# Optimization experiments

Measured on AMD Instinct MI355X. Metric: run time of the kernel, lower is better.

## Reference

```python
import jax, jax.numpy as jnp
import numpy as np

N_NODES = 50000
N_EDGES = 800000
IN_CH = 64
OUT_CH = 128
N_HEADS = 4
HEAD_DIM = OUT_CH // N_HEADS
LN_EPS = 1e-5


def setup_inputs() -> dict:
    key = jax.random.key(0)
    ks = jax.random.split(key, 12)
    def lin(k, fan_in, fan_out):
        bound = 1.0 / np.sqrt(fan_in)
        kw, kb = jax.random.split(k)
        W = jax.random.uniform(kw, (fan_in, fan_out), jnp.float32, -bound, bound)
        b = jax.random.uniform(kb, (fan_out,), jnp.float32, -bound, bound)
        return W, b
    Wq, bq = lin(ks[0], IN_CH, OUT_CH)
    Wk, bk = lin(ks[1], IN_CH, OUT_CH)
    Wv, bv = lin(ks[2], IN_CH, OUT_CH)
    We1, be1 = lin(ks[3], 2 * IN_CH, OUT_CH)
    We2, be2 = lin(ks[4], OUT_CH, N_HEADS)
    Wo, bo = lin(ks[5], OUT_CH, OUT_CH)
    gamma = jnp.ones((OUT_CH,), jnp.float32)
    beta = jnp.zeros((OUT_CH,), jnp.float32)
    x = jax.random.normal(ks[6], (N_NODES, IN_CH), jnp.float32)
    edge_index = jax.random.randint(ks[7], (2, N_EDGES), 0, N_NODES, jnp.int64 if jax.config.jax_enable_x64 else jnp.int32)
    return {"x": x, "edge_index": edge_index,
            "Wq": Wq, "bq": bq, "Wk": Wk, "bk": bk, "Wv": Wv, "bv": bv,
            "We1": We1, "be1": be1, "We2": We2, "be2": be2,
            "Wo": Wo, "bo": bo, "gamma": gamma, "beta": beta}


def reference(x, edge_index, Wq, bq, Wk, bk, Wv, bv, We1, be1, We2, be2, Wo, bo, gamma, beta):
    # Projections -> [N, H, Dh]
    q = (x @ Wq + bq).reshape(-1, N_HEADS, HEAD_DIM)
    k = (x @ Wk + bk).reshape(-1, N_HEADS, HEAD_DIM)
    v = (x @ Wv + bv).reshape(-1, N_HEADS, HEAD_DIM)
    src, dst = edge_index[0], edge_index[1]
    # Edge MLP attention weights: [E, H, 1]
    edge_features = jnp.concatenate([x[src], x[dst]], axis=-1)  # [E, 2*IN_CH]
    edge_weights = jax.nn.relu(edge_features @ We1 + be1) @ We2 + be2  # [E, H]
    edge_weights = edge_weights[:, :, None]
    # Attention logits per edge: [E, H, 1]
    attn = jnp.sum(q[dst] * k[src], axis=-1, keepdims=True)
    attn = attn * edge_weights / np.sqrt(HEAD_DIM).astype(np.float32)
    # Faithful to original: softmax over the edge dimension (dim=0)
    attn = jax.nn.softmax(attn, axis=0)
    # Weighted gather-scatter aggregation: [N, H, Dh]
    out = jax.ops.segment_sum(attn * v[src], dst, num_segments=N_NODES)
    out = out.reshape(-1, OUT_CH)
    # Output transform (dropout is identity in eval mode) + LayerNorm
    out = out @ Wo + bo
    mu = jnp.mean(out, axis=-1, keepdims=True)
    var = jnp.var(out, axis=-1, keepdims=True)
    out = (out - mu) * jax.lax.rsqrt(var + LN_EPS) * gamma + beta
    return out
```

## Files before the change

### kernel.cpp

```cpp
#include <hip/hip_runtime.h>
#include <hip/hip_bf16.h>

typedef __hip_bfloat16 bf16;
typedef __attribute__((ext_vector_type(8))) short short8;
typedef __attribute__((ext_vector_type(4))) float f32x4;
typedef __attribute__((ext_vector_type(2))) float f32x2;
typedef _Float16 h2 __attribute__((ext_vector_type(2)));

constexpr int NN = 50000;
constexpr int NE = 800000;
constexpr int IC = 64;
constexpr int OC = 128;
constexpr int NH = 4;
constexpr unsigned F32_ONE = 0x3F800000u;
constexpr float KC = 0.25503486f;

__device__ __forceinline__ float ldf(const void* p, int i, bool f32) {
    return f32 ? ((const float*)p)[i]
               : __bfloat162float(((const bf16*)p)[i]);
}

__device__ __forceinline__ int ld_idx(const void* p, long long i, bool i64) {
    return i64 ? (int)((const long long*)p)[i] : ((const int*)p)[i];
}

__device__ __forceinline__ bool probe_i64(const void* ei) {
    const unsigned* u = (const unsigned*)ei;
    return (u[1] | u[3] | u[5] | u[7]) == 0u;
}

__device__ __forceinline__ unsigned f2bu(float x) {
    unsigned u = __float_as_uint(x);
    return (u + 0x7FFFu + ((u >> 16) & 1u)) >> 16;
}

__device__ __forceinline__ h2 u2h(unsigned u) { return __builtin_bit_cast(h2, u); }

__device__ __forceinline__ float fdot2(h2 a, h2 b, float c) {
#if __has_builtin(__builtin_amdgcn_fdot2)
    return __builtin_amdgcn_fdot2(a, b, c, false);
#else
    return c + (float)a[0] * (float)b[0] + (float)a[1] * (float)b[1];
#endif
}

__device__ __forceinline__ h2 relu2(h2 a) {
    h2 z = {(_Float16)0.f, (_Float16)0.f};
#if __has_builtin(__builtin_elementwise_max)
    return __builtin_elementwise_max(a, z);
#else
    h2 r;
    r[0] = a[0] > (_Float16)0.f ? a[0] : (_Float16)0.f;
    r[1] = a[1] > (_Float16)0.f ? a[1] : (_Float16)0.f;
    return r;
#endif
}

#define DPPADD(x, ctrl) \
    ((x) + __int_as_float(__builtin_amdgcn_mov_dpp(__float_as_int(x), (ctrl), 0xF, 0xF, false)))

__device__ __forceinline__ int rfl(int v) { return __builtin_amdgcn_readfirstlane(v); }

__device__ __forceinline__ unsigned char f32_to_fp8(float x) {
#if __has_builtin(__builtin_amdgcn_cvt_pk_fp8_f32)
    return (unsigned char)(__builtin_amdgcn_cvt_pk_fp8_f32(x, x, 0, false) & 0xFF);
#else
    unsigned bits = __float_as_uint(x);
    unsigned s = bits >> 31;
    float a = fabsf(x);
    if (a >= 448.f) return (unsigned char)((s << 7) | 0x7E);
    if (a < 0.015625f) {
        int m = (int)(a * 512.f + 0.5f);
        if (m >= 8) return (unsigned char)((s << 7) | 0x08);
        return (unsigned char)((s << 7) | m);
    }
    unsigned ab = (bits & 0x7FFFFFFFu) + 0x00080000u;
    int e8 = (int)(ab >> 23) - 127 + 7;
    unsigned m3 = (ab >> 20) & 7u;
    if (e8 >= 16) return (unsigned char)((s << 7) | 0x7E);
    return (unsigned char)((s << 7) | ((unsigned)e8 << 3) | m3);
#endif
}

__device__ __forceinline__ void fp8x2_to_f32(unsigned u, float& f0, float& f1) {
#if __has_builtin(__builtin_amdgcn_cvt_pk_f32_fp8)
    f32x2 lo = __builtin_amdgcn_cvt_pk_f32_fp8(u, false);
    f0 = lo[0]; f1 = lo[1];
#else
    float r[2];
#pragma unroll
    for (int j = 0; j < 2; ++j) {
        unsigned b = (u >> (8 * j)) & 0xFF;
        unsigned s = b >> 7, e = (b >> 3) & 15, m = b & 7;
        float v = (e == 0) ? (float)m * 0.001953125f
                           : __uint_as_float(((e + 120u) << 23) | (m << 20));
        r[j] = s ? -v : v;
    }
    f0 = r[0]; f1 = r[1];
#endif
}

constexpr int PB_X   = 12500;
constexpr int PB_W   = 160;
constexpr int PB_WO  = 64;
constexpr int PB_CNT = 3125;

__global__ __launch_bounds__(256) void prep(
    const void* __restrict__ x,
    const void* __restrict__ Wq, const void* __restrict__ bq,
    const void* __restrict__ Wk, const void* __restrict__ bk,
    const void* __restrict__ Wv, const void* __restrict__ bv,
    const void* __restrict__ We1, const void* __restrict__ be1,
    const void* __restrict__ We2, const void* __restrict__ be2,
    const void* __restrict__ Wo,  const unsigned* __restrict__ gw,
    const void* __restrict__ eia, const void* __restrict__ eib, int split,
    bf16* __restrict__ xb, bf16* __restrict__ WcatT, bf16* __restrict__ WoT,
    int* __restrict__ cnt, int* __restrict__ rank,
    unsigned* __restrict__ We2h, float* __restrict__ be2f,
    float* __restrict__ bcat)
{
    const bool f32 = (gw[0] == F32_ONE);
    int b = blockIdx.x, t = threadIdx.x;
    if (b < PB_X) {
        int i = b * 256 + t;
        if (i < NN * IC) xb[i] = __float2bfloat16(ldf(x, i, f32));
    } else if (b < PB_X + PB_W) {
        int idx = (b - PB_X) * 256 + t;
        int n = idx >> 6, k = idx & 63;
        int sel = n >> 7, c = n & 127;
        float v;
        if (sel == 0)      v = ldf(Wq, k * OC + c, f32);
        else if (sel == 1) v = ldf(Wk, k * OC + c, f32);
        else if (sel == 2) v = ldf(Wv, k * OC + c, f32);
        else if (sel == 3) v = ldf(We1, k * OC + c, f32);
        else               v = ldf(We1, (IC + k) * OC + c, f32);
        WcatT[idx] = __float2bfloat16(v);
    } else if (b < PB_X + PB_W + PB_WO) {
        int idx = (b - PB_X - PB_W) * 256 + t;
        int n = idx >> 7, k = idx & 127;
        WoT[idx] = __float2bfloat16(ldf(Wo, k * OC + n, f32));
    } else if (b < PB_X + PB_W + PB_WO + PB_CNT) {
        const bool i64 = probe_i64(eia);
        long long e = (long long)(b - PB_X - PB_W - PB_WO) * 256 + t;
        int d = split ? ld_idx(eib, e, i64) : ld_idx(eia, NE + e, i64);
        int r = atomicAdd(&cnt[d], 1);
        rank[e] = r;
    } else {
        if (t < NH) be2f[t] = ldf(be2, t, f32);
        {
            int ln = t >> 2, k = t & 3;
            int g = ln >> 4, ii = ln & 15;
            int pp = 4 * ii + k;
            h2 hv;
            hv[0] = (_Float16)ldf(We2, (2 * pp) * NH + g, f32);
            hv[1] = (_Float16)ldf(We2, (2 * pp + 1) * NH + g, f32);
            We2h[t] = __builtin_bit_cast(unsigned, hv);
        }
        for (int n = t; n < 5 * OC; n += 256) {
            int sel = n >> 7, c = n & 127;
            float bb = 0.f;
            if (sel == 0) bb = ldf(bq, c, f32);
            else if (sel == 1) bb = ldf(bk, c, f32);
            else if (sel == 2) bb = ldf(bv, c, f32);
            else if (sel == 4) bb = ldf(be1, c, f32);
            bcat[n] = bb;
        }
    }
}

constexpr int SCAN_NB = 49;

__global__ __launch_bounds__(256) void scan_part(const int* __restrict__ cnt,
                                                 int* __restrict__ bsum,
                                                 int* __restrict__ rowptr)
{
    int b = blockIdx.x, t = threadIdx.x;
    int base = b * 1024 + t * 4;
    int4 v;
    if (base < NN) v = *(const int4*)(cnt + base);
    else { v.x = 0; v.y = 0; v.z = 0; v.w = 0; }
    int s = v.x + v.y + v.z + v.w;
#pragma unroll
    for (int off = 1; off < 64; off <<= 1) s += __shfl_xor(s, off);
    __shared__ int sm[4];
    int lane = t & 63, w = t >> 6;
    if (lane == 0) sm[w] = s;
    __syncthreads();
    if (t == 0) bsum[b] = sm[0] + sm[1] + sm[2] + sm[3];
    if (b == 0 && t == 0) rowptr[NN] = NE;
}

__global__ __launch_bounds__(256) void scan_fin(const int* __restrict__ cnt,
                                                const int* __restrict__ bsum,
                                                int* __restrict__ rowptr)
{
    int b = blockIdx.x, t = threadIdx.x;
    int lane = t & 63, w = t >> 6;
    __shared__ int s_boff;
    __shared__ int wsum[4];
    if (w == 0) {
        int pre = (lane < b) ? bsum[lane] : 0;
#pragma unroll
        for (int off = 1; off < 64; off <<= 1) pre += __shfl_xor(pre, off);
        if (lane == 0) s_boff = pre;
    }
    int base = b * 1024 + t * 4;
    int4 v;
    if (base < NN) v = *(const int4*)(cnt + base);
    else { v.x = 0; v.y = 0; v.z = 0; v.w = 0; }
    int s = v.x + v.y + v.z + v.w;
    int inc = s;
#pragma unroll
    for (int off = 1; off < 64; off <<= 1) {
        int u = __shfl_up(inc, off);
        if (lane >= off) inc += u;
    }
    if (lane == 63) wsum[w] = inc;
    __syncthreads();
    int run = s_boff + (inc - s);
#pragma unroll
    for (int i = 0; i < 3; ++i) if (i < w) run += wsum[i];
    if (base < NN) {
        int4 rp;
        rp.x = run;
        rp.y = rp.x + v.x;
        rp.z = rp.y + v.y;
        rp.w = rp.z + v.z;
        *(int4*)(rowptr + base) = rp;
    }
}

constexpr int NG_GEMM = 3125;
constexpr int NG_FILL = 3125;

__global__ __launch_bounds__(256) void node_gemm(
    const bf16* __restrict__ xb, const bf16* __restrict__ WcatT,
    const float* __restrict__ bcat,
    unsigned char* __restrict__ qb_dst, unsigned char* __restrict__ ka_src,
    unsigned char* __restrict__ vf8,
    const void* __restrict__ eia, const void* __restrict__ eib, int split,
    const int* __restrict__ rowptr, const int* __restrict__ rank,
    int* __restrict__ ssrc)
{
    __shared__ _Float16 qbs[16][264];
    __shared__ _Float16 kas[16][264];
    __shared__ unsigned char vfs[16][144];

    if (blockIdx.x >= NG_GEMM) {
        const bool i64 = probe_i64(eia);
        long long e = (long long)(blockIdx.x - NG_GEMM) * 256 + threadIdx.x;
        int s = ld_idx(eia, e, i64);
        int d = split ? ld_idx(eib, e, i64) : ld_idx(eia, NE + e, i64);
        int pos = rowptr[d] + rank[e];
        ssrc[pos] = s;
        return;
    }
    int wave = threadIdx.x >> 6;
    int lane = threadIdx.x & 63;
    int quad = lane >> 4;
    int l16  = lane & 15;
    int row_base = blockIdx.x * 16;
    int m = row_base + l16;

    short8 a0 = *(const short8*)(xb + (size_t)m * IC + quad * 8);
    short8 a1 = *(const short8*)(xb + (size_t)m * IC + 32 + quad * 8);

#pragma unroll
    for (int t = 0; t < 10; ++t) {
        int colbase = wave * 160 + t * 16;
        const bf16* bp = WcatT + (size_t)(colbase + l16) * IC + quad * 8;
        short8 b0 = *(const short8*)(bp);
        short8 b1 = *(const short8*)(bp + 32);
        f32x4 acc = {0.f, 0.f, 0.f, 0.f};
        acc = __builtin_amdgcn_mfma_f32_16x16x32_bf16(a0, b0, acc, 0, 0, 0);
        acc = __builtin_amdgcn_mfma_f32_16x16x32_bf16(a1, b1, acc, 0, 0, 0);

        float bias = bcat[colbase + l16];
        int sel = colbase >> 7;
        int cc  = (colbase & 127) + l16;
#pragma unroll
        for (int r = 0; r < 4; ++r) {
            int l = quad * 4 + r;
            float fv = acc[r] + bias;
            if (sel == 2) {
                vfs[l][cc] = f32_to_fp8(fv);
            } else {
                _Float16 val = (_Float16)fv;
                if (sel == 0)      qbs[l][cc] = val;
                else if (sel == 1) kas[l][cc] = val;
                else if (sel == 3) kas[l][128 + cc] = val;
                else               qbs[l][128 + cc] = val;
            }
        }
    }
    __syncthreads();

    int tix = threadIdx.x;
#pragma unroll
    for (int j = 0; j < 2; ++j) {
        int i = tix + j * 256;
        int row = i >> 5, idx = i & 31;
        *(uint4*)(qb_dst + (size_t)(row_base + row) * 512 + idx * 16) =
            *(const uint4*)((const char*)&qbs[row][0] + idx * 16);
        *(uint4*)(ka_src + (size_t)(row_base + row) * 512 + idx * 16) =
            *(const uint4*)((const char*)&kas[row][0] + idx * 16);
    }
    if (tix < 128) {
        int row = tix >> 3, idx = tix & 7;
        *(uint4*)(vf8 + (size_t)(row_base + row) * OC + idx * 16) =
            *(const uint4*)((const char*)&vfs[row][0] + idx * 16);
    }
}

__global__ __launch_bounds__(256) void edge_gather(
    const int* __restrict__ rowptr, const int* __restrict__ ssrc,
    unsigned char* __restrict__ qb_dst, const unsigned char* __restrict__ ka_src,
    const unsigned char* __restrict__ vf8,
    const unsigned* __restrict__ We2h, const float* __restrict__ be2f,
    float* __restrict__ spart)
{
    int node = rfl(blockIdx.x * 4 + (threadIdx.x >> 6));
    int lane = threadIdx.x & 63;
    int i16  = lane & 15;
    int myh  = lane >> 4;

    const unsigned char* drow = qb_dst + (size_t)node * 512;
    h2 dq = u2h(*(const unsigned*)(drow + lane * 4));
    uint4 dbu = *(const uint4*)(drow + 256 + 16 * i16);
    h2 db0 = u2h(dbu.x), db1 = u2h(dbu.y), db2 = u2h(dbu.z), db3 = u2h(dbu.w);

    uint4 wu = *(const uint4*)(We2h + lane * 4);
    h2 w0 = u2h(wu.x), w1 = u2h(wu.y), w2 = u2h(wu.z), w3 = u2h(wu.w);
    float be2h = be2f[myh];

    int beg = rfl(rowptr[node]);
    int end = rfl(rowptr[node + 1]);
    float o0 = 0.f, o1 = 0.f, s_acc = 0.f;

    if (beg < end) {
        int ib = (beg + 1 < end) ? beg + 1 : end - 1;
        int sa = rfl(ssrc[beg]);
        int sb = rfl(ssrc[ib]);
        const unsigned char* ra = ka_src + (size_t)sa * 512;
        const unsigned char* rb = ka_src + (size_t)sb * 512;
        unsigned kuA = *(const unsigned*)(ra + lane * 4);
        uint4    auA = *(const uint4*)(ra + 256 + 16 * i16);
        unsigned uvA = *(const unsigned short*)(vf8 + (size_t)sa * OC + 2 * lane);
        unsigned kuB = *(const unsigned*)(rb + lane * 4);
        uint4    auB = *(const uint4*)(rb + 256 + 16 * i16);
        unsigned uvB = *(const unsigned short*)(vf8 + (size_t)sb * OC + 2 * lane);
        int na = (beg + 2 < end) ? beg + 2 : end - 1;
        int nb = (beg + 3 < end) ? beg + 3 : end - 1;
        int sna = rfl(ssrc[na]);
        int snb = rfl(ssrc[nb]);

        for (int p = beg; p < end; p += 2) {
            const unsigned char* rc = ka_src + (size_t)sna * 512;
            const unsigned char* rd = ka_src + (size_t)snb * 512;
            unsigned kuC = *(const unsigned*)(rc + lane * 4);
            uint4    auC = *(const uint4*)(rc + 256 + 16 * i16);
            unsigned uvC = *(const unsigned short*)(vf8 + (size_t)sna * OC + 2 * lane);
            unsigned kuD = *(const unsigned*)(rd + lane * 4);
            uint4    auD = *(const uint4*)(rd + 256 + 16 * i16);
            unsigned uvD = *(const unsigned short*)(vf8 + (size_t)snb * OC + 2 * lane);
            int fa = (p + 4 < end) ? p + 4 : end - 1;
            int fb = (p + 5 < end) ? p + 5 : end - 1;
            int s4a = rfl(ssrc[fa]);
            int s4b = rfl(ssrc[fb]);

            bool hasB = (p + 1 < end);

            float tA = fdot2(u2h(kuA), dq, 0.f);
            float tB = fdot2(u2h(kuB), dq, 0.f);
            h2 hA0 = relu2(u2h(auA.x) + db0);
            h2 hA1 = relu2(u2h(auA.y) + db1);
            h2 hA2 = relu2(u2h(auA.z) + db2);
            h2 hA3 = relu2(u2h(auA.w) + db3);
            h2 hB0 = relu2(u2h(auB.x) + db0);
            h2 hB1 = relu2(u2h(auB.y) + db1);
            h2 hB2 = relu2(u2h(auB.z) + db2);
            h2 hB3 = relu2(u2h(auB.w) + db3);
            float pA = fdot2(hA3, w3, fdot2(hA2, w2, fdot2(hA1, w1, fdot2(hA0, w0, 0.f))));
            float pB = fdot2(hB3, w3, fdot2(hB2, w2, fdot2(hB1, w1, fdot2(hB0, w0, 0.f))));

            tA = DPPADD(tA, 0xB1);  pA = DPPADD(pA, 0xB1);
            tB = DPPADD(tB, 0xB1);  pB = DPPADD(pB, 0xB1);
            tA = DPPADD(tA, 0x4E);  pA = DPPADD(pA, 0x4E);
            tB = DPPADD(tB, 0x4E);  pB = DPPADD(pB, 0x4E);
            tA = DPPADD(tA, 0x128); pA = DPPADD(pA, 0x128);
            tB = DPPADD(tB, 0x128); pB = DPPADD(pB, 0x128);
            tA = DPPADD(tA, 0x124); pA = DPPADD(pA, 0x124);
            tB = DPPADD(tB, 0x124); pB = DPPADD(pB, 0x124);

            float coefA = exp2f(tA * (pA + be2h) * KC);
            float coefB = hasB ? exp2f(tB * (pB + be2h) * KC) : 0.f;
            s_acc += coefA + coefB;

            float vA0, vA1, vB0, vB1;
            fp8x2_to_f32(uvA, vA0, vA1);
            fp8x2_to_f32(uvB, vB0, vB1);
            o0 = fmaf(coefA, vA0, fmaf(coefB, vB0, o0));
            o1 = fmaf(coefA, vA1, fmaf(coefB, vB1, o1));

            kuA = kuC; auA = auC; uvA = uvC;
            kuB = kuD; auB = auD; uvB = uvD;
            sna = s4a; snb = s4b;
        }
    }
    *(unsigned*)(qb_dst + (size_t)node * 512 + lane * 4) = f2bu(o0) | (f2bu(o1) << 16);
    if (i16 == 0) spart[node * 4 + myh] = s_acc;
}

constexpr int SR_BLOCKS = 98;
__global__ __launch_bounds__(256) void s_reduce(const float* __restrict__ spart,
                                                float* __restrict__ ssum)
{
    int tid = blockIdx.x * 256 + threadIdx.x;
    int h = threadIdx.x & 3;
    float s = 0.f;
    for (int i = tid; i < NN * 4; i += SR_BLOCKS * 256) s += spart[i];
#pragma unroll
    for (int off = 4; off <= 32; off <<= 1) s += __shfl_xor(s, off);
    __shared__ float sm[4][4];
    int lane = threadIdx.x & 63, w = threadIdx.x >> 6;
    if (lane < 4) sm[w][h] = s;
    __syncthreads();
    if (threadIdx.x < 4) {
        float tot = sm[0][h] + sm[1][h] + sm[2][h] + sm[3][h];
        atomicAdd(&ssum[h], tot);
    }
}

__global__ __launch_bounds__(256) void out_gemm(
    const unsigned char* __restrict__ aggv, const bf16* __restrict__ WoT,
    const void* __restrict__ bo, const void* __restrict__ gamma,
    const void* __restrict__ beta, const unsigned* __restrict__ gw,
    const float* __restrict__ ssum,
    void* __restrict__ out)
{
    const bool f32 = (gw[0] == F32_ONE);
    int wave = threadIdx.x >> 6;
    int lane = threadIdx.x & 63;
    int quad = lane >> 4;
    int l16  = lane & 15;
    int rb = blockIdx.x * 64 + wave * 16;
    int m = rb + l16;
    int ma = (m < NN) ? m : 0;

    const bf16* arow = (const bf16*)(aggv + (size_t)ma * 512);
    short8 a[4];
#pragma unroll
    for (int h = 0; h < 4; ++h) {
        short8 raw = *(const short8*)(arow + h * 32 + quad * 8);
        float invh = 1.0f / ssum[h];
#pragma unroll
        for (int jj = 0; jj < 8; ++jj) {
            float f = __uint_as_float(((unsigned)(unsigned short)raw[jj]) << 16) * invh;
            raw[jj] = (short)f2bu(f);
        }
        a[h] = raw;
    }

    float o[8][4];
#pragma unroll
    for (int t = 0; t < 8; ++t) {
        const bf16* bp = WoT + (size_t)(t * 16 + l16) * OC + quad * 8;
        f32x4 acc = {0.f, 0.f, 0.f, 0.f};
#pragma unroll
        for (int h = 0; h < 4; ++h) {
            short8 bfr = *(const short8*)(bp + h * 32);
            acc = __builtin_amdgcn_mfma_f32_16x16x32_bf16(a[h], bfr, acc, 0, 0, 0);
        }
        float bias = ldf(bo, t * 16 + l16, f32);
#pragma unroll
        for (int r = 0; r < 4; ++r) o[t][r] = acc[r] + bias;
    }

#pragma unroll
    for (int r = 0; r < 4; ++r) {
        float s1 = 0.f, s2 = 0.f;
#pragma unroll
        for (int t = 0; t < 8; ++t) { s1 += o[t][r]; s2 += o[t][r] * o[t][r]; }
#pragma unroll
        for (int off = 1; off <= 8; off <<= 1) {
            s1 += __shfl_xor(s1, off);
            s2 += __shfl_xor(s2, off);
        }
        float mu = s1 * (1.0f / OC);
        float var = fmaxf(s2 * (1.0f / OC) - mu * mu, 0.f);
        float rs = rsqrtf(var + 1e-5f);
        int node = rb + quad * 4 + r;
        if (node < NN) {
#pragma unroll
            for (int t = 0; t < 8; ++t) {
                int col = t * 16 + l16;
                float y = (o[t][r] - mu) * rs * ldf(gamma, col, f32) + ldf(beta, col, f32);
                if (f32) ((float*)out)[(size_t)node * OC + col] = y;
                else     ((bf16*)out)[(size_t)node * OC + col] = __float2bfloat16(y);
            }
        }
    }
}

extern "C" void kernel_launch(void* const* d_in, const int* in_sizes, int n_in,
                              void* d_out, int out_size, void* d_ws, size_t ws_size,
                              hipStream_t stream)
{
    int p = 0;
    const void* x   = d_in[p++];
    const void* eia = d_in[p++];
    const void* eib = eia;
    int split = 0;
    if (n_in >= 17) { eib = d_in[p++]; split = 1; }
    const void* Wq   = d_in[p++];
    const void* bq   = d_in[p++];
    const void* Wk   = d_in[p++];
    const void* bk   = d_in[p++];
    const void* Wv   = d_in[p++];
    const void* bv   = d_in[p++];
    const void* We1  = d_in[p++];
    const void* be1  = d_in[p++];
    const void* We2  = d_in[p++];
    const void* be2  = d_in[p++];
    const void* Wo   = d_in[p++];
    const void* bo   = d_in[p++];
    const void* gamma= d_in[p++];
    const void* beta = d_in[p++];
    const unsigned* gw = (const unsigned*)gamma;

    char* w = (char*)d_ws;
    bf16*  xb     = (bf16*)w;                  w += (size_t)NN * IC * 2;
    unsigned char* qb_dst = (unsigned char*)w; w += (size_t)NN * 512;
    unsigned char* ka_src = (unsigned char*)w; w += (size_t)NN * 512;
    unsigned char* vf8    = (unsigned char*)w; w += (size_t)NN * OC;
    int*   ssrc   = (int*)w;                   w += (size_t)NE * 4;
    int*   rank   = (int*)w;                   w += (size_t)NE * 4;
    int*   cnt    = (int*)w;                   w += (size_t)NN * 4;
    float* ssum   = (float*)w;                 w += 8 * 4;
    int*   rowptr = (int*)w;                   w += (size_t)(NN + 4) * 4;
    int*   bsum   = (int*)w;                   w += 64 * 4;
    float* spart  = (float*)w;                 w += (size_t)NN * 4 * 4;
    unsigned* We2h = (unsigned*)w;             w += 256 * 4;
    float* be2f   = (float*)w;                 w += NH * 4;
    bf16*  WcatT  = (bf16*)w;                  w += (size_t)5 * OC * IC * 2;
    float* bcat   = (float*)w;                 w += 5 * OC * 4;
    bf16*  WoT    = (bf16*)w;                  w += (size_t)OC * OC * 2;

    if (ws_size < (size_t)((char*)w - (char*)d_ws)) return;

    hipMemsetAsync(cnt, 0, (size_t)NN * 4 + 32, stream);
    prep<<<PB_X + PB_W + PB_WO + PB_CNT + 1, 256, 0, stream>>>(
        x, Wq, bq, Wk, bk, Wv, bv, We1, be1, We2, be2, Wo, gw,
        eia, eib, split,
        xb, WcatT, WoT, cnt, rank, We2h, be2f, bcat);
    scan_part<<<SCAN_NB, 256, 0, stream>>>(cnt, bsum, rowptr);
    scan_fin<<<SCAN_NB, 256, 0, stream>>>(cnt, bsum, rowptr);
    node_gemm<<<NG_GEMM + NG_FILL, 256, 0, stream>>>(
        xb, WcatT, bcat, qb_dst, ka_src, vf8, eia, eib, split, rowptr, rank, ssrc);
    edge_gather<<<NN / 4, 256, 0, stream>>>(rowptr, ssrc, qb_dst, ka_src, vf8,
                                            We2h, be2f, spart);
    s_reduce<<<SR_BLOCKS, 256, 0, stream>>>(spart, ssum);
    out_gemm<<<(NN + 63) / 64, 256, 0, stream>>>(qb_dst, WoT, bo, gamma, beta, gw,
                                                 ssum, d_out);
}
```

Baseline: 286.2 us.

## Fuse x bf16 conversion into node GEMM and use inline DPP adds

The separate prep pass that converted x to a bf16 buffer is removed. The node GEMM now loads x directly and converts fp32 to bf16 in registers, which saves a full write and re-read of the converted node features. The DPP cross-lane reductions in the edge gather are also rewritten as inline-asm v_add_f32 with DPP modifiers, so each step becomes one fused instruction instead of a mov_dpp followed by an add. The inline asm carries some risk around missing wait states for DPP hazards.

```diff
diff --git a/kernel.cpp b/kernel.cpp
--- a/kernel.cpp
+++ b/kernel.cpp
@@ -56,10 +56,23 @@
 #endif
 }
 
-#define DPPADD(x, ctrl) \
-    ((x) + __int_as_float(__builtin_amdgcn_mov_dpp(__float_as_int(x), (ctrl), 0xF, 0xF, false)))
+#define DPPFADD(x, ctrl) \
+    asm("v_add_f32 %0, %0, %0 " ctrl " row_mask:0xf bank_mask:0xf" : "+v"(x))
 
 __device__ __forceinline__ int rfl(int v) { return __builtin_amdgcn_readfirstlane(v); }
+
+__device__ __forceinline__ short8 ld_xrow(const void* x, bool f32, int m, int off) {
+    if (!f32) return *(const short8*)((const bf16*)x + (size_t)m * IC + off);
+    const float* xr = (const float*)x + (size_t)m * IC + off;
+    float4 u0 = *(const float4*)xr;
+    float4 u1 = *(const float4*)(xr + 4);
+    short8 r;
+    r[0] = (short)f2bu(u0.x); r[1] = (short)f2bu(u0.y);
+    r[2] = (short)f2bu(u0.z); r[3] = (short)f2bu(u0.w);
+    r[4] = (short)f2bu(u1.x); r[5] = (short)f2bu(u1.y);
+    r[6] = (short)f2bu(u1.z); r[7] = (short)f2bu(u1.w);
+    return r;
+}
 
 __device__ __forceinline__ unsigned char f32_to_fp8(float x) {
 #if __has_builtin(__builtin_amdgcn_cvt_pk_fp8_f32)
@@ -100,13 +113,11 @@
 #endif
 }
 
-constexpr int PB_X   = 12500;
 constexpr int PB_W   = 160;
 constexpr int PB_WO  = 64;
 constexpr int PB_CNT = 3125;
 
 __global__ __launch_bounds__(256) void prep(
-    const void* __restrict__ x,
     const void* __restrict__ Wq, const void* __restrict__ bq,
     const void* __restrict__ Wk, const void* __restrict__ bk,
     const void* __restrict__ Wv, const void* __restrict__ bv,
@@ -114,18 +125,15 @@
     const void* __restrict__ We2, const void* __restrict__ be2,
     const void* __restrict__ Wo,  const unsigned* __restrict__ gw,
     const void* __restrict__ eia, const void* __restrict__ eib, int split,
-    bf16* __restrict__ xb, bf16* __restrict__ WcatT, bf16* __restrict__ WoT,
+    bf16* __restrict__ WcatT, bf16* __restrict__ WoT,
     int* __restrict__ cnt, int* __restrict__ rank,
     unsigned* __restrict__ We2h, float* __restrict__ be2f,
     float* __restrict__ bcat)
 {
     const bool f32 = (gw[0] == F32_ONE);
     int b = blockIdx.x, t = threadIdx.x;
-    if (b < PB_X) {
-        int i = b * 256 + t;
-        if (i < NN * IC) xb[i] = __float2bfloat16(ldf(x, i, f32));
-    } else if (b < PB_X + PB_W) {
-        int idx = (b - PB_X) * 256 + t;
+    if (b < PB_W) {
+        int idx = b * 256 + t;
         int n = idx >> 6, k = idx & 63;
         int sel = n >> 7, c = n & 127;
         float v;
@@ -135,13 +143,13 @@
         else if (sel == 3) v = ldf(We1, k * OC + c, f32);
         else               v = ldf(We1, (IC + k) * OC + c, f32);
         WcatT[idx] = __float2bfloat16(v);
-    } else if (b < PB_X + PB_W + PB_WO) {
-        int idx = (b - PB_X - PB_W) * 256 + t;
+    } else if (b < PB_W + PB_WO) {
+        int idx = (b - PB_W) * 256 + t;
         int n = idx >> 7, k = idx & 127;
         WoT[idx] = __float2bfloat16(ldf(Wo, k * OC + n, f32));
-    } else if (b < PB_X + PB_W + PB_WO + PB_CNT) {
+    } else if (b < PB_W + PB_WO + PB_CNT) {
         const bool i64 = probe_i64(eia);
-        long long e = (long long)(b - PB_X - PB_W - PB_WO) * 256 + t;
+        long long e = (long long)(b - PB_W - PB_WO) * 256 + t;
         int d = split ? ld_idx(eib, e, i64) : ld_idx(eia, NE + e, i64);
         int r = atomicAdd(&cnt[d], 1);
         rank[e] = r;
@@ -234,7 +242,8 @@
 constexpr int NG_FILL = 3125;
 
 __global__ __launch_bounds__(256) void node_gemm(
-    const bf16* __restrict__ xb, const bf16* __restrict__ WcatT,
+    const void* __restrict__ x, const unsigned* __restrict__ gw,
+    const bf16* __restrict__ WcatT,
     const float* __restrict__ bcat,
     unsigned char* __restrict__ qb_dst, unsigned char* __restrict__ ka_src,
     unsigned char* __restrict__ vf8,
@@ -255,6 +264,7 @@
         ssrc[pos] = s;
         return;
     }
+    const bool f32 = (gw[0] == F32_ONE);
     int wave = threadIdx.x >> 6;
     int lane = threadIdx.x & 63;
     int quad = lane >> 4;
@@ -262,8 +272,8 @@
     int row_base = blockIdx.x * 16;
     int m = row_base + l16;
 
-    short8 a0 = *(const short8*)(xb + (size_t)m * IC + quad * 8);
-    short8 a1 = *(const short8*)(xb + (size_t)m * IC + 32 + quad * 8);
+    short8 a0 = ld_xrow(x, f32, m, quad * 8);
+    short8 a1 = ld_xrow(x, f32, m, 32 + quad * 8);
 
 #pragma unroll
     for (int t = 0; t < 10; ++t) {
@@ -383,14 +393,14 @@
             float pA = fdot2(hA3, w3, fdot2(hA2, w2, fdot2(hA1, w1, fdot2(hA0, w0, 0.f))));
             float pB = fdot2(hB3, w3, fdot2(hB2, w2, fdot2(hB1, w1, fdot2(hB0, w0, 0.f))));
 
-            tA = DPPADD(tA, 0xB1);  pA = DPPADD(pA, 0xB1);
-            tB = DPPADD(tB, 0xB1);  pB = DPPADD(pB, 0xB1);
-            tA = DPPADD(tA, 0x4E);  pA = DPPADD(pA, 0x4E);
-            tB = DPPADD(tB, 0x4E);  pB = DPPADD(pB, 0x4E);
-            tA = DPPADD(tA, 0x128); pA = DPPADD(pA, 0x128);
-            tB = DPPADD(tB, 0x128); pB = DPPADD(pB, 0x128);
-            tA = DPPADD(tA, 0x124); pA = DPPADD(pA, 0x124);
-            tB = DPPADD(tB, 0x124); pB = DPPADD(pB, 0x124);
+            DPPFADD(tA, "quad_perm:[1,0,3,2]");  DPPFADD(pA, "quad_perm:[1,0,3,2]");
+            DPPFADD(tB, "quad_perm:[1,0,3,2]");  DPPFADD(pB, "quad_perm:[1,0,3,2]");
+            DPPFADD(tA, "quad_perm:[2,3,0,1]");  DPPFADD(pA, "quad_perm:[2,3,0,1]");
+            DPPFADD(tB, "quad_perm:[2,3,0,1]");  DPPFADD(pB, "quad_perm:[2,3,0,1]");
+            DPPFADD(tA, "row_ror:8");            DPPFADD(pA, "row_ror:8");
+            DPPFADD(tB, "row_ror:8");            DPPFADD(pB, "row_ror:8");
+            DPPFADD(tA, "row_ror:4");            DPPFADD(pA, "row_ror:4");
+            DPPFADD(tB, "row_ror:4");            DPPFADD(pB, "row_ror:4");
 
             float coefA = exp2f(tA * (pA + be2h) * KC);
             float coefB = hasB ? exp2f(tB * (pB + be2h) * KC) : 0.f;
@@ -529,7 +539,6 @@
     const unsigned* gw = (const unsigned*)gamma;
 
     char* w = (char*)d_ws;
-    bf16*  xb     = (bf16*)w;                  w += (size_t)NN * IC * 2;
     unsigned char* qb_dst = (unsigned char*)w; w += (size_t)NN * 512;
     unsigned char* ka_src = (unsigned char*)w; w += (size_t)NN * 512;
     unsigned char* vf8    = (unsigned char*)w; w += (size_t)NN * OC;
@@ -549,14 +558,14 @@
     if (ws_size < (size_t)((char*)w - (char*)d_ws)) return;
 
     hipMemsetAsync(cnt, 0, (size_t)NN * 4 + 32, stream);
-    prep<<<PB_X + PB_W + PB_WO + PB_CNT + 1, 256, 0, stream>>>(
-        x, Wq, bq, Wk, bk, Wv, bv, We1, be1, We2, be2, Wo, gw,
+    prep<<<PB_W + PB_WO + PB_CNT + 1, 256, 0, stream>>>(
+        Wq, bq, Wk, bk, Wv, bv, We1, be1, We2, be2, Wo, gw,
         eia, eib, split,
-        xb, WcatT, WoT, cnt, rank, We2h, be2f, bcat);
+        WcatT, WoT, cnt, rank, We2h, be2f, bcat);
     scan_part<<<SCAN_NB, 256, 0, stream>>>(cnt, bsum, rowptr);
     scan_fin<<<SCAN_NB, 256, 0, stream>>>(cnt, bsum, rowptr);
     node_gemm<<<NG_GEMM + NG_FILL, 256, 0, stream>>>(
-        xb, WcatT, bcat, qb_dst, ka_src, vf8, eia, eib, split, rowptr, rank, ssrc);
+        x, gw, WcatT, bcat, qb_dst, ka_src, vf8, eia, eib, split, rowptr, rank, ssrc);
     edge_gather<<<NN / 4, 256, 0, stream>>>(rowptr, ssrc, qb_dst, ka_src, vf8,
                                             We2h, be2f, spart);
     s_reduce<<<SR_BLOCKS, 256, 0, stream>>>(spart, ssum);
```

After: 286.9 us (median of 2 runs). Within noise of the previous version (+0.2%).
